# Kernel tuning notes

Hardware: AMD Instinct MI355X
Metric: run time of the kernel (lower is better)

Reference implementation:

```python
import math
import jax, jax.numpy as jnp
import numpy as np

N_LAYERS = 6
N_HEADS = 8
WINDOW = 4
LN_EPS = 1e-6


def _get_rel_emb(emb, length):
    # emb: [1, 2*WINDOW+1, kc] -> [1, 2*length-1, kc]
    max_rel = 2 * WINDOW + 1
    pad = max(0, length - (WINDOW + 1))
    start = max(0, WINDOW + 1 - length)
    end = max_rel + 2 * length - 1
    if pad > 0:
        emb = jnp.pad(emb, ((0, 0), (pad, pad), (0, 0)))
    return emb[:, start:end]


def _rel_to_abs(x):
    # x: [b,h,l,2l-1] -> [b,h,l,l]
    b, h, l, _ = x.shape
    x = jnp.pad(x, ((0, 0), (0, 0), (0, 0), (0, 1)))
    xf = x.reshape(b, h, l * 2 * l)
    xf = jnp.pad(xf, ((0, 0), (0, 0), (0, l - 1)))
    return xf.reshape(b, h, l + 1, 2 * l - 1)[:, :, :l, l - 1:]


def _abs_to_rel(x):
    # x: [b,h,l,l] -> [b,h,l,2l-1]
    b, h, l, _ = x.shape
    x = jnp.pad(x, ((0, 0), (0, 0), (0, 0), (0, l - 1)))
    xf = x.reshape(b, h, -1)
    xf = jnp.pad(xf, ((0, 0), (0, 0), (l, 0)))
    return xf.reshape(b, h, l, 2 * l)[..., 1:]


def _layer_norm(x, scale, bias):
    m = jnp.mean(x, axis=-1, keepdims=True)
    v = jnp.mean(jnp.square(x - m), axis=-1, keepdims=True)
    return (x - m) * jax.lax.rsqrt(v + LN_EPS) * scale + bias


def _forward(x, x_mask, Wq, bq, Wk, bk, Wv, bv, Wo, bo, emb_rel_k, emb_rel_v,
             ln1_scale, ln1_bias, W1, b1, W2, b2, ln2_scale, ln2_bias):
    B, T, C = x.shape
    H = N_HEADS
    KC = C // H
    scale = 1.0 / math.sqrt(KC)
    attn_mask = x_mask[:, :, None, :] * x_mask[:, :, :, None]  # [B,1,T,T]
    mask_t = jnp.transpose(x_mask, (0, 2, 1))  # [B,T,1]
    x = x * mask_t
    for l in range(N_LAYERS):
        # --- relative-position multi-head self-attention ---
        q = (x @ Wq[l] + bq[l]).reshape(B, T, H, KC).transpose(0, 2, 1, 3)
        k = (x @ Wk[l] + bk[l]).reshape(B, T, H, KC).transpose(0, 2, 1, 3)
        v = (x @ Wv[l] + bv[l]).reshape(B, T, H, KC).transpose(0, 2, 1, 3)
        scores = jnp.einsum('bhqd,bhkd->bhqk', q * scale, k)
        rk = _get_rel_emb(emb_rel_k[l], T)[0]  # [2T-1, KC] (heads shared)
        rel_logits = jnp.einsum('bhld,md->bhlm', q * scale, rk)
        scores = scores + _rel_to_abs(rel_logits)
        scores = jnp.where(attn_mask == 0, -10000.0, scores)
        p = jax.nn.softmax(scores, axis=-1)
        out = jnp.einsum('bhqk,bhkd->bhqd', p, v)
        rv = _get_rel_emb(emb_rel_v[l], T)[0]
        out = out + jnp.einsum('bhlm,md->bhld', _abs_to_rel(p), rv)
        out = out.transpose(0, 2, 1, 3).reshape(B, T, C)
        y = out @ Wo[l] + bo[l]
        x = _layer_norm(x + y, ln1_scale[l], ln1_bias[l])
        # --- pointwise conv FFN (kernel_size=1) ---
        h1 = jax.nn.relu((x * mask_t) @ W1[l] + b1[l])
        y = (h1 * mask_t) @ W2[l] + b2[l]
        y = y * mask_t
        x = _layer_norm(x + y, ln2_scale[l], ln2_bias[l])
    return x * mask_t


def setup_inputs() -> dict:
    key = jax.random.key(0)
    B, T, C, F, L, H = 8, 768, 512, 2048, N_LAYERS, N_HEADS
    KC = C // H
    ks = jax.random.split(key, 10)
    nrm = lambda k, s, sd=0.02: jax.random.normal(k, s, jnp.float32) * sd
    return {
        'x': jax.random.normal(ks[0], (B, T, C), jnp.float32),
        'x_mask': jnp.ones((B, 1, T), jnp.float32),
        'Wq': nrm(ks[1], (L, C, C)), 'bq': jnp.zeros((L, C), jnp.float32),
        'Wk': nrm(ks[2], (L, C, C)), 'bk': jnp.zeros((L, C), jnp.float32),
        'Wv': nrm(ks[3], (L, C, C)), 'bv': jnp.zeros((L, C), jnp.float32),
        'Wo': nrm(ks[4], (L, C, C)), 'bo': jnp.zeros((L, C), jnp.float32),
        'emb_rel_k': nrm(ks[5], (L, 1, 2 * WINDOW + 1, KC), KC ** -0.5),
        'emb_rel_v': nrm(ks[6], (L, 1, 2 * WINDOW + 1, KC), KC ** -0.5),
        'ln1_scale': jnp.ones((L, C), jnp.float32), 'ln1_bias': jnp.zeros((L, C), jnp.float32),
        'W1': nrm(ks[7], (L, C, F)), 'b1': jnp.zeros((L, F), jnp.float32),
        'W2': nrm(ks[8], (L, F, C)), 'b2': jnp.zeros((L, C), jnp.float32),
        'ln2_scale': jnp.ones((L, C), jnp.float32), 'ln2_bias': jnp.zeros((L, C), jnp.float32),
    }


def reference(x, x_mask, Wq, bq, Wk, bk, Wv, bv, Wo, bo, emb_rel_k, emb_rel_v,
              ln1_scale, ln1_bias, W1, b1, W2, b2, ln2_scale, ln2_bias):
    return _forward(x, x_mask, Wq, bq, Wk, bk, Wv, bv, Wo, bo, emb_rel_k, emb_rel_v,
                    ln1_scale, ln1_bias, W1, b1, W2, b2, ln2_scale, ln2_bias)
```

## Files before the change

### kernel.cpp

```cpp
#include <hip/hip_runtime.h>
#include <stdint.h>


typedef unsigned short u16;
typedef __attribute__((ext_vector_type(8))) __bf16 bf16x8;
typedef __attribute__((ext_vector_type(4))) float f32x4;

#define B_ 8
#define T_ 768
#define C_ 512
#define F_ 2048
#define LOG2E 1.4426950408889634f

__device__ __forceinline__ float b2f(u16 u) {
    union { float f; uint32_t i; } x; x.i = ((uint32_t)u) << 16; return x.f;
}
__device__ __forceinline__ u16 f2b(float f) {
    union { float f; uint32_t i; } x; x.f = f;
    return (u16)((x.i + 0x7fffu + ((x.i >> 16) & 1u)) >> 16);
}

template <int EPI>
__global__ __launch_bounds__(256) void gemm_bt4(
    const u16* __restrict__ A, int aStride,
    const u16* __restrict__ Bt, int bStride,
    const float* __restrict__ bias,
    u16* __restrict__ out, int oStride, int K, float epiScale)
{
    const int tid = threadIdx.x;
    const int wave = tid >> 6, lane = tid & 63;
    const int wm = wave & 1, wn = wave >> 1;
    const int quad = lane >> 4, l16 = lane & 15;
    const int m0 = blockIdx.x * 64;
    const int n0 = blockIdx.y * 64;

    __shared__ u16 As[64 * 64];
    __shared__ u16 Bs[64 * 64];

    const f32x4 vzero = {0.f, 0.f, 0.f, 0.f};
    f32x4 acc[2][2];
#pragma unroll
    for (int i = 0; i < 2; ++i)
#pragma unroll
        for (int j = 0; j < 2; ++j) acc[i][j] = vzero;

    for (int k0 = 0; k0 < K; k0 += 64) {
#pragma unroll
        for (int i = 0; i < 2; ++i) {
            int c = tid + i * 256;
            int row = c >> 3, pc = c & 7, lc = pc ^ (row & 7);
            *(uint4*)&As[c * 8] =
                *(const uint4*)(A + (long long)(m0 + row) * aStride + (k0 + lc * 8));
            *(uint4*)&Bs[c * 8] =
                *(const uint4*)(Bt + (long long)(n0 + row) * bStride + (k0 + lc * 8));
        }
        __syncthreads();
        __builtin_amdgcn_s_setprio(1);
#pragma unroll
        for (int ks = 0; ks < 2; ++ks) {
            bf16x8 af[2], bfr[2];
#pragma unroll
            for (int mi = 0; mi < 2; ++mi) {
                int row = wm * 32 + mi * 16 + l16;
                int pc = ((ks << 2) | quad) ^ (row & 7);
                af[mi] = *(const bf16x8*)&As[row * 64 + pc * 8];
            }
#pragma unroll
            for (int ni = 0; ni < 2; ++ni) {
                int row = wn * 32 + ni * 16 + l16;
                int pc = ((ks << 2) | quad) ^ (row & 7);
                bfr[ni] = *(const bf16x8*)&Bs[row * 64 + pc * 8];
            }
#pragma unroll
            for (int mi = 0; mi < 2; ++mi)
#pragma unroll
                for (int ni = 0; ni < 2; ++ni)
                    acc[mi][ni] = __builtin_amdgcn_mfma_f32_16x16x32_bf16(
                        bfr[ni], af[mi], acc[mi][ni], 0, 0, 0);
        }
        __builtin_amdgcn_s_setprio(0);
        __syncthreads();
    }

#pragma unroll
    for (int mi = 0; mi < 2; ++mi) {
        int row = m0 + wm * 32 + mi * 16 + l16;
#pragma unroll
        for (int ni = 0; ni < 2; ++ni) {
            int colb = n0 + wn * 32 + ni * 16 + quad * 4;
            u16 pk[4];
#pragma unroll
            for (int r = 0; r < 4; ++r) {
                float v = acc[mi][ni][r] + bias[colb + r];
                if (EPI == 1) v = v > 0.f ? v : 0.f;
                if (EPI == 3) { if (colb + r < 512) v *= epiScale; }
                pk[r] = f2b(v);
            }
            uint2 p;
            p.x = (uint32_t)pk[0] | ((uint32_t)pk[1] << 16);
            p.y = (uint32_t)pk[2] | ((uint32_t)pk[3] << 16);
            *(uint2*)(out + (long long)row * oStride + colb) = p;
        }
    }
}

__global__ __launch_bounds__(256) void bandg_k(
    const u16* __restrict__ qkv, const float* __restrict__ erk,
    float* __restrict__ bandg)
{
    __shared__ float erkS[576];
    const int tid = threadIdx.x;
    for (int idx = tid; idx < 576; idx += 256) erkS[idx] = erk[idx];
    __syncthreads();
    const int gid = blockIdx.x * 256 + tid;
    const int row = gid >> 3, h = gid & 7;
    const u16* q = qkv + (long long)row * 1536 + h * 64;
    float acc[9];
#pragma unroll
    for (int e = 0; e < 9; ++e) acc[e] = 0.f;
#pragma unroll
    for (int c = 0; c < 8; ++c) {
        uint4 d4 = *(const uint4*)(q + c * 8);
        const uint32_t dw[4] = {d4.x, d4.y, d4.z, d4.w};
#pragma unroll
        for (int j = 0; j < 8; ++j) {
            u16 uu = (u16)((dw[j >> 1] >> ((j & 1) * 16)) & 0xffff);
            float qv = b2f(uu);
            int d = c * 8 + j;
#pragma unroll
            for (int e = 0; e < 9; ++e) acc[e] += qv * erkS[e * 64 + d];
        }
    }
    float* o = bandg + (long long)gid * 9;
#pragma unroll
    for (int e = 0; e < 9; ++e) o[e] = acc[e];
}

__global__ __launch_bounds__(128) void flash_attn(
    const u16* __restrict__ qkv, const u16* __restrict__ vt,
    const float* __restrict__ mask, const float* __restrict__ bandg,
    const float* __restrict__ erv, u16* __restrict__ outb)
{
    const int tid = threadIdx.x;
    const int w = tid >> 6, lane = tid & 63;
    const int quad = lane >> 4, l16 = lane & 15;
    const int orig = blockIdx.y * 24 + blockIdx.x;
    const int swz = (orig & 7) * 192 + (orig >> 3);
    const int qt = swz % 24, bh = swz / 24;
    const int b = bh >> 3, h = bh & 7;
    const int q0 = qt * 32;

    __shared__ u16 Ql[32 * 64];
    __shared__ u16 Kt[64 * 64];
    __shared__ u16 Vt[64 * 64];
    __shared__ u16 Pl[2][16 * 64];
    __shared__ float bandk[32][10];
    __shared__ float maskK[64];

#pragma unroll
    for (int i = 0; i < 2; ++i) {
        int c = tid + i * 128;
        int r = c >> 3, pc = c & 7, lc = pc ^ (r & 7);
        *(uint4*)&Ql[c * 8] =
            *(const uint4*)(qkv + (long long)(b * T_ + q0 + r) * 1536 + h * 64 + lc * 8);
    }
    for (int idx = tid; idx < 288; idx += 128) {
        int r = idx / 9, e = idx - r * 9;
        bandk[r][e] = bandg[((long long)(b * T_ + q0 + r) * 8 + h) * 9 + e];
    }

    const int i_row = q0 + w * 16 + l16;
    const float mi = mask[b * T_ + i_row];
    float m_run = -1e30f, l_run = 0.f;
    const f32x4 vzero = {0.f, 0.f, 0.f, 0.f};
    f32x4 vacc[4] = {vzero, vzero, vzero, vzero};
    float pb[3] = {0.f, 0.f, 0.f};

    __syncthreads();
    bf16x8 qf[2];
#pragma unroll
    for (int ks = 0; ks < 2; ++ks) {
        int r = w * 16 + l16;
        int pc = ((ks << 2) | quad) ^ (r & 7);
        qf[ks] = *(const bf16x8*)&Ql[r * 64 + pc * 8];
    }

    for (int kt = 0; kt < 12; ++kt) {
        __syncthreads();
#pragma unroll
        for (int i = 0; i < 4; ++i) {
            int c = tid + i * 128;
            int r = c >> 3, pc = c & 7, lc = pc ^ (r & 7);
            *(uint4*)&Kt[c * 8] =
                *(const uint4*)(qkv + (long long)(b * T_ + kt * 64 + r) * 1536 + 512 + h * 64 + lc * 8);
            *(uint4*)&Vt[c * 8] =
                *(const uint4*)(vt + ((long long)bh * 64 + r) * T_ + kt * 64 + lc * 8);
        }
        if (tid < 64) maskK[tid] = mask[b * T_ + kt * 64 + tid];
        __syncthreads();

        const float mkv = maskK[lane];
        const bool tile_clean = (__ballot(mkv == 0.f) == 0ull);
        const bool fast = tile_clean && (mi != 0.f);
        const bool has_band = (kt * 64 <= q0 + w * 16 + 19) &&
                              (kt * 64 + 67 >= q0 + w * 16);

        f32x4 sacc[4];
#pragma unroll
        for (int ni = 0; ni < 4; ++ni) sacc[ni] = vzero;
        __builtin_amdgcn_s_setprio(1);
#pragma unroll
        for (int ks = 0; ks < 2; ++ks)
#pragma unroll
            for (int ni = 0; ni < 4; ++ni) {
                int r = ni * 16 + l16;
                int pc = ((ks << 2) | quad) ^ (r & 7);
                bf16x8 kf = *(const bf16x8*)&Kt[r * 64 + pc * 8];
                sacc[ni] = __builtin_amdgcn_mfma_f32_16x16x32_bf16(kf, qf[ks], sacc[ni], 0, 0, 0);
            }
        __builtin_amdgcn_s_setprio(0);

        if (has_band) {
#pragma unroll
            for (int ni = 0; ni < 4; ++ni)
#pragma unroll
                for (int r = 0; r < 4; ++r) {
                    int jl = ni * 16 + quad * 4 + r;
                    int dlt = kt * 64 + jl - i_row;
                    if (dlt >= -4 && dlt <= 4)
                        sacc[ni][r] += bandk[w * 16 + l16][dlt + 4];
                }
        }
        if (!fast) {
#pragma unroll
            for (int ni = 0; ni < 4; ++ni)
#pragma unroll
                for (int r = 0; r < 4; ++r) {
                    int jl = ni * 16 + quad * 4 + r;
                    if (mi * maskK[jl] == 0.f) sacc[ni][r] = -14427.0f;
                }
        }

        float mx;
        {
            float a0 = fmaxf(sacc[0][0], sacc[0][1]), a1 = fmaxf(sacc[0][2], sacc[0][3]);
            float b0 = fmaxf(sacc[1][0], sacc[1][1]), b1 = fmaxf(sacc[1][2], sacc[1][3]);
            float c0 = fmaxf(sacc[2][0], sacc[2][1]), c1 = fmaxf(sacc[2][2], sacc[2][3]);
            float d0 = fmaxf(sacc[3][0], sacc[3][1]), d1 = fmaxf(sacc[3][2], sacc[3][3]);
            float t0 = fmaxf(fmaxf(a0, a1), fmaxf(b0, b1));
            float t1 = fmaxf(fmaxf(c0, c1), fmaxf(d0, d1));
            mx = fmaxf(t0, t1);
        }
        mx = fmaxf(mx, __shfl_xor(mx, 16));
        mx = fmaxf(mx, __shfl_xor(mx, 32));
        const float m_new = fmaxf(m_run, mx);
        const float alpha = exp2f(m_run - m_new);
        m_run = m_new;
        l_run *= alpha;
#pragma unroll
        for (int ni = 0; ni < 4; ++ni) vacc[ni] = vacc[ni] * alpha;
#pragma unroll
        for (int k = 0; k < 3; ++k) pb[k] *= alpha;

        float lsum = 0.f;
#pragma unroll
        for (int ni = 0; ni < 4; ++ni) {
            float u0 = exp2f(sacc[ni][0] - m_new);
            float u1 = exp2f(sacc[ni][1] - m_new);
            float u2 = exp2f(sacc[ni][2] - m_new);
            float u3 = exp2f(sacc[ni][3] - m_new);
            lsum += (u0 + u1) + (u2 + u3);
            union { __bf16 h[2]; uint32_t u; } cA, cB;
            cA.h[0] = (__bf16)u0; cA.h[1] = (__bf16)u1;
            cB.h[0] = (__bf16)u2; cB.h[1] = (__bf16)u3;
            int c0 = ni * 16 + quad * 4;
            int phys = (((c0 >> 3) ^ (l16 & 7)) << 3) + (c0 & 7);
            uint2 p; p.x = cA.u; p.y = cB.u;
            *(uint2*)&Pl[w][l16 * 64 + phys] = p;
        }
        l_run += lsum;

        if (has_band) {
#pragma unroll
            for (int k = 0; k < 3; ++k) {
                int e = quad * 3 + k;
                if (e < 9) {
                    int jl = i_row + e - 4 - kt * 64;
                    if (jl >= 0 && jl < 64) {
                        int phys = (((jl >> 3) ^ (l16 & 7)) << 3) + (jl & 7);
                        pb[k] += b2f(Pl[w][l16 * 64 + phys]);
                    }
                }
            }
        }

        __builtin_amdgcn_s_setprio(1);
#pragma unroll
        for (int ks = 0; ks < 2; ++ks) {
            int pcc = ((ks << 2) | quad) ^ (l16 & 7);
            bf16x8 pf = *(const bf16x8*)&Pl[w][l16 * 64 + pcc * 8];
#pragma unroll
            for (int ni = 0; ni < 4; ++ni) {
                int r = ni * 16 + l16;
                int pc = ((ks << 2) | quad) ^ (r & 7);
                bf16x8 vf = *(const bf16x8*)&Vt[r * 64 + pc * 8];
                vacc[ni] = __builtin_amdgcn_mfma_f32_16x16x32_bf16(vf, pf, vacc[ni], 0, 0, 0);
            }
        }
        __builtin_amdgcn_s_setprio(0);
    }

    l_run += __shfl_xor(l_run, 16);
    l_run += __shfl_xor(l_run, 32);
    const float rinv = 1.f / l_run;

    float pband[9];
#pragma unroll
    for (int e = 0; e < 9; ++e) {
        float val = (quad == e / 3) ? pb[e % 3] : 0.f;
        val += __shfl_xor(val, 16);
        val += __shfl_xor(val, 32);
        pband[e] = val * rinv;
    }

    u16* orow = outb + (long long)(b * T_ + i_row) * C_ + h * 64;
#pragma unroll
    for (int ni = 0; ni < 4; ++ni) {
        u16 pk[4];
#pragma unroll
        for (int r = 0; r < 4; ++r) {
            int d = ni * 16 + quad * 4 + r;
            float v = vacc[ni][r] * rinv;
#pragma unroll
            for (int e = 0; e < 9; ++e) v += pband[e] * erv[e * 64 + d];
            pk[r] = f2b(v);
        }
        uint2 p;
        p.x = (uint32_t)pk[0] | ((uint32_t)pk[1] << 16);
        p.y = (uint32_t)pk[2] | ((uint32_t)pk[3] << 16);
        *(uint2*)(orow + ni * 16 + quad * 4) = p;
    }
}

__global__ void transpose_qkvo(const float* __restrict__ Wq, const float* __restrict__ Wk,
                               const float* __restrict__ Wv, const float* __restrict__ Wo,
                               u16* __restrict__ wqkvT, u16* __restrict__ woT)
{
    __shared__ u16 tile[32][33];
    const int z = blockIdx.z, l = z >> 2, which = z & 3;
    const float* src = (which == 0 ? Wq : which == 1 ? Wk : which == 2 ? Wv : Wo)
                       + (long long)l * 262144;
    u16* dst = (which == 3) ? woT + (long long)l * 262144
                            : wqkvT + (long long)l * 786432 + which * 262144;
    const int r0 = blockIdx.y * 32, c0 = blockIdx.x * 32;
    const int tx = threadIdx.x, ty = threadIdx.y;
#pragma unroll
    for (int i = 0; i < 32; i += 8)
        tile[ty + i][tx] = f2b(src[(long long)(r0 + ty + i) * 512 + (c0 + tx)]);
    __syncthreads();
#pragma unroll
    for (int i = 0; i < 32; i += 8)
        dst[(long long)(c0 + ty + i) * 512 + (r0 + tx)] = tile[tx][ty + i];
}

__global__ void transpose_f2bL(const float* __restrict__ src0, int sStride, long long sLayer,
                               u16* __restrict__ dst0, int dStride, long long dLayer)
{
    __shared__ u16 tile[32][33];
    const int l = blockIdx.z;
    const float* src = src0 + (long long)l * sLayer;
    u16* dst = dst0 + (long long)l * dLayer;
    const int r0 = blockIdx.y * 32, c0 = blockIdx.x * 32;
    const int tx = threadIdx.x, ty = threadIdx.y;
#pragma unroll
    for (int i = 0; i < 32; i += 8)
        tile[ty + i][tx] = f2b(src[(long long)(r0 + ty + i) * sStride + (c0 + tx)]);
    __syncthreads();
#pragma unroll
    for (int i = 0; i < 32; i += 8)
        dst[(long long)(c0 + ty + i) * dStride + (r0 + tx)] = tile[tx][ty + i];
}

__global__ void transpose_b(const u16* __restrict__ src, long long sB1, long long sB2, int sStride,
                            u16* __restrict__ dst, long long dB1, long long dB2, int dStride)
{
    __shared__ u16 tile[32][33];
    const int z = blockIdx.z, zb = z >> 3, zh = z & 7;
    src += (long long)zb * sB1 + (long long)zh * sB2;
    dst += (long long)zb * dB1 + (long long)zh * dB2;
    const int r0 = blockIdx.y * 32, c0 = blockIdx.x * 32;
    const int tx = threadIdx.x, ty = threadIdx.y;
#pragma unroll
    for (int i = 0; i < 32; i += 8)
        tile[ty + i][tx] = src[(long long)(r0 + ty + i) * sStride + (c0 + tx)];
    __syncthreads();
#pragma unroll
    for (int i = 0; i < 32; i += 8)
        dst[(long long)(c0 + ty + i) * dStride + (r0 + tx)] = tile[tx][ty + i];
}

__global__ void concat_bias(const float* __restrict__ bq, const float* __restrict__ bk,
                            const float* __restrict__ bv, float* __restrict__ dst)
{
    int i = blockIdx.x * 256 + threadIdx.x;
    int l = i / 1536, n = i - l * 1536;
    float v = (n < 512) ? bq[l * 512 + n]
             : (n < 1024 ? bk[l * 512 + (n - 512)] : bv[l * 512 + (n - 1024)]);
    dst[i] = v;
}

__global__ void mask_in(const float* __restrict__ x, const float* __restrict__ mask,
                        u16* __restrict__ out)
{
    int i4 = (blockIdx.x * 256 + threadIdx.x) * 4;
    float4 xv = *(const float4*)(x + i4);
    float m = mask[i4 >> 9];
    u16 pk[4] = {f2b(xv.x * m), f2b(xv.y * m), f2b(xv.z * m), f2b(xv.w * m)};
    uint2 p; p.x = (uint32_t)pk[0] | ((uint32_t)pk[1] << 16);
    p.y = (uint32_t)pk[2] | ((uint32_t)pk[3] << 16);
    *(uint2*)(out + i4) = p;
}

__global__ void mask_out(const u16* __restrict__ x, const float* __restrict__ mask,
                         float* __restrict__ out)
{
    int i4 = (blockIdx.x * 256 + threadIdx.x) * 4;
    uint2 p = *(const uint2*)(x + i4);
    float m = mask[i4 >> 9];
    float4 o;
    o.x = b2f((u16)(p.x & 0xffff)) * m;
    o.y = b2f((u16)(p.x >> 16)) * m;
    o.z = b2f((u16)(p.y & 0xffff)) * m;
    o.w = b2f((u16)(p.y >> 16)) * m;
    *(float4*)(out + i4) = o;
}

__global__ __launch_bounds__(256) void add_ln(
    const u16* __restrict__ x, const u16* __restrict__ y,
    const float* __restrict__ sc, const float* __restrict__ bi,
    u16* __restrict__ outx)
{
    const int wave = threadIdx.x >> 6, lane = threadIdx.x & 63;
    const long long r = (long long)blockIdx.x * 4 + wave;
    const u16* xr = x + r * C_;
    const u16* yr = y + r * C_;
    float v[8], s = 0.f;
#pragma unroll
    for (int it = 0; it < 2; ++it) {
        int j0 = it * 256 + lane * 4;
        uint2 px = *(const uint2*)(xr + j0);
        uint2 py = *(const uint2*)(yr + j0);
        v[it * 4 + 0] = b2f((u16)(px.x & 0xffff)) + b2f((u16)(py.x & 0xffff));
        v[it * 4 + 1] = b2f((u16)(px.x >> 16))    + b2f((u16)(py.x >> 16));
        v[it * 4 + 2] = b2f((u16)(px.y & 0xffff)) + b2f((u16)(py.y & 0xffff));
        v[it * 4 + 3] = b2f((u16)(px.y >> 16))    + b2f((u16)(py.y >> 16));
        s += v[it * 4 + 0] + v[it * 4 + 1] + v[it * 4 + 2] + v[it * 4 + 3];
    }
#pragma unroll
    for (int off = 32; off > 0; off >>= 1) s += __shfl_down(s, off);
    s = __shfl(s, 0);
    const float mean = s * (1.f / 512.f);
    float var = 0.f;
#pragma unroll
    for (int l = 0; l < 8; ++l) { float d = v[l] - mean; var += d * d; }
#pragma unroll
    for (int off = 32; off > 0; off >>= 1) var += __shfl_down(var, off);
    var = __shfl(var, 0);
    const float rs = rsqrtf(var * (1.f / 512.f) + 1e-6f);
    u16* orow = outx + r * C_;
#pragma unroll
    for (int it = 0; it < 2; ++it) {
        int j0 = it * 256 + lane * 4;
        float4 s4 = *(const float4*)(sc + j0);
        float4 b4 = *(const float4*)(bi + j0);
        u16 pk[4];
        pk[0] = f2b((v[it * 4 + 0] - mean) * rs * s4.x + b4.x);
        pk[1] = f2b((v[it * 4 + 1] - mean) * rs * s4.y + b4.y);
        pk[2] = f2b((v[it * 4 + 2] - mean) * rs * s4.z + b4.z);
        pk[3] = f2b((v[it * 4 + 3] - mean) * rs * s4.w + b4.w);
        uint2 p; p.x = (uint32_t)pk[0] | ((uint32_t)pk[1] << 16);
        p.y = (uint32_t)pk[2] | ((uint32_t)pk[3] << 16);
        *(uint2*)(orow + j0) = p;
    }
}

extern "C" void kernel_launch(void* const* d_in, const int* in_sizes, int n_in,
                              void* d_out, int out_size, void* d_ws, size_t ws_size,
                              hipStream_t stream)
{
    const float* x    = (const float*)d_in[0];
    const float* mask = (const float*)d_in[1];
    const float* Wq   = (const float*)d_in[2];
    const float* bq   = (const float*)d_in[3];
    const float* Wk   = (const float*)d_in[4];
    const float* bk   = (const float*)d_in[5];
    const float* Wv   = (const float*)d_in[6];
    const float* bv   = (const float*)d_in[7];
    const float* Wo   = (const float*)d_in[8];
    const float* bo   = (const float*)d_in[9];
    const float* erk  = (const float*)d_in[10];
    const float* erv  = (const float*)d_in[11];
    const float* ln1s = (const float*)d_in[12];
    const float* ln1b = (const float*)d_in[13];
    const float* W1   = (const float*)d_in[14];
    const float* b1   = (const float*)d_in[15];
    const float* W2   = (const float*)d_in[16];
    const float* b2   = (const float*)d_in[17];
    const float* ln2s = (const float*)d_in[18];
    const float* ln2b = (const float*)d_in[19];
    float* out = (float*)d_out;
    u16* ws  = (u16*)d_ws;

    const long long CF = 512LL * 2048;
    const int M = B_ * T_;

    u16* wqkvT   = ws;
    u16* woT     = ws + 4718592;
    u16* w1T     = ws + 6291456;
    u16* w2T     = ws + 12582912;
    float* bqkv  = (float*)(ws + 18874368);
    u16* xb      = ws + 18892800;
    u16* qkvb    = ws + 22038528;
    u16* vtb     = ws + 31475712;
    u16* attnb   = ws + 34621440;
    u16* scr     = ws + 37767168;
    float* bandg = (float*)(ws + 50350080);
    u16* yb      = vtb;

    const dim3 tb(32, 8);

    transpose_qkvo<<<dim3(16, 16, 24), tb, 0, stream>>>(Wq, Wk, Wv, Wo, wqkvT, woT);
    transpose_f2bL<<<dim3(64, 16, 6), tb, 0, stream>>>(W1, 2048, CF, w1T, 512, 1048576);
    transpose_f2bL<<<dim3(16, 64, 6), tb, 0, stream>>>(W2, 512,  CF, w2T, 2048, 1048576);
    concat_bias<<<36, 256, 0, stream>>>(bq, bk, bv, bqkv);
    mask_in<<<(M * 512) / 1024, 256, 0, stream>>>(x, mask, xb);

    for (int l = 0; l < 6; ++l) {
        gemm_bt4<3><<<dim3(96, 24), 256, 0, stream>>>(
            xb, 512, wqkvT + (long long)l * 786432, 512, bqkv + l * 1536,
            qkvb, 1536, 512, 0.125f * LOG2E);
        bandg_k<<<192, 256, 0, stream>>>(qkvb, erk + l * 576, bandg);
        transpose_b<<<dim3(2, 24, 64), tb, 0, stream>>>(
            qkvb + 1024, 768LL * 1536, 64, 1536,
            vtb, 8LL * 64 * 768, 64LL * 768, 768);
        flash_attn<<<dim3(24, 64), 128, 0, stream>>>(
            qkvb, vtb, mask, bandg, erv + l * 576, attnb);
        gemm_bt4<0><<<dim3(96, 8), 256, 0, stream>>>(
            attnb, 512, woT + (long long)l * 262144, 512, bo + l * 512,
            yb, 512, 512, 0.f);
        add_ln<<<1536, 256, 0, stream>>>(xb, yb, ln1s + l * 512, ln1b + l * 512, xb);
        gemm_bt4<1><<<dim3(96, 32), 256, 0, stream>>>(
            xb, 512, w1T + (long long)l * 1048576, 512, b1 + l * 2048,
            scr, 2048, 512, 0.f);
        gemm_bt4<0><<<dim3(96, 8), 256, 0, stream>>>(
            scr, 2048, w2T + (long long)l * 1048576, 2048, b2 + l * 512,
            yb, 512, 2048, 0.f);
        add_ln<<<1536, 256, 0, stream>>>(xb, yb, ln2s + l * 512, ln2b + l * 512, xb);
    }

    mask_out<<<(M * 512) / 1024, 256, 0, stream>>>(xb, mask, out);
}
```

Baseline: 1.017 ms.

## Load K/V fragments directly from global memory in single-wave attention blocks

The attention kernel changes from two-wave blocks that stage K and V tiles in shared memory to one-wave blocks of 16 query rows. Each lane reads its K and V MFMA fragments straight from global memory, which removes the per-tile block barriers and LDS copies. The cost is that each K/V tile is fetched twice as often, once per 16-row block instead of once per 32 rows, so the kernel leans on L2/L1 cache hits. Row-mask handling now uses a wave ballot, and mask values go to LDS only on the slow path.

```diff
diff --git a/kernel.cpp b/kernel.cpp
--- a/kernel.cpp
+++ b/kernel.cpp
@@ -136,74 +136,60 @@
     for (int e = 0; e < 9; ++e) o[e] = acc[e];
 }
 
-__global__ __launch_bounds__(128) void flash_attn(
+__global__ __launch_bounds__(64) void flash_attn(
     const u16* __restrict__ qkv, const u16* __restrict__ vt,
     const float* __restrict__ mask, const float* __restrict__ bandg,
     const float* __restrict__ erv, u16* __restrict__ outb)
 {
-    const int tid = threadIdx.x;
-    const int w = tid >> 6, lane = tid & 63;
+    const int lane = threadIdx.x;
     const int quad = lane >> 4, l16 = lane & 15;
-    const int orig = blockIdx.y * 24 + blockIdx.x;
-    const int swz = (orig & 7) * 192 + (orig >> 3);
-    const int qt = swz % 24, bh = swz / 24;
+    const int orig = blockIdx.y * 48 + blockIdx.x;
+    const int swz = (orig & 7) * 384 + (orig >> 3);
+    const int qt = swz % 48, bh = swz / 48;
     const int b = bh >> 3, h = bh & 7;
-    const int q0 = qt * 32;
-
-    __shared__ u16 Ql[32 * 64];
-    __shared__ u16 Kt[64 * 64];
-    __shared__ u16 Vt[64 * 64];
-    __shared__ u16 Pl[2][16 * 64];
-    __shared__ float bandk[32][10];
-    __shared__ float maskK[64];
-
-#pragma unroll
-    for (int i = 0; i < 2; ++i) {
-        int c = tid + i * 128;
-        int r = c >> 3, pc = c & 7, lc = pc ^ (r & 7);
-        *(uint4*)&Ql[c * 8] =
-            *(const uint4*)(qkv + (long long)(b * T_ + q0 + r) * 1536 + h * 64 + lc * 8);
-    }
-    for (int idx = tid; idx < 288; idx += 128) {
+    const int q0 = qt * 16;
+
+    __shared__ u16 Pl[16 * 64];
+    __shared__ float bandk[16][10];
+    __shared__ float maskW[64];
+
+    for (int idx = lane; idx < 144; idx += 64) {
         int r = idx / 9, e = idx - r * 9;
         bandk[r][e] = bandg[((long long)(b * T_ + q0 + r) * 8 + h) * 9 + e];
     }
-
-    const int i_row = q0 + w * 16 + l16;
+    __syncthreads();
+
+    const int i_row = q0 + l16;
     const float mi = mask[b * T_ + i_row];
+    const bool row_masked_any = (__ballot(mi == 0.f) != 0ull);
+
+    const u16* qrow = qkv + (long long)(b * T_ + i_row) * 1536 + h * 64;
+    bf16x8 qf[2];
+#pragma unroll
+    for (int ks = 0; ks < 2; ++ks)
+        qf[ks] = *(const bf16x8*)(qrow + ks * 32 + quad * 8);
+
+    const u16* kbase[4];
+    const u16* vbase[4];
+#pragma unroll
+    for (int ni = 0; ni < 4; ++ni) {
+        int r = ni * 16 + l16;
+        kbase[ni] = qkv + ((long long)(b * T_) + r) * 1536 + 512 + h * 64;
+        vbase[ni] = vt + ((long long)bh * 64 + r) * T_;
+    }
+
     float m_run = -1e30f, l_run = 0.f;
     const f32x4 vzero = {0.f, 0.f, 0.f, 0.f};
     f32x4 vacc[4] = {vzero, vzero, vzero, vzero};
     float pb[3] = {0.f, 0.f, 0.f};
 
-    __syncthreads();
-    bf16x8 qf[2];
-#pragma unroll
-    for (int ks = 0; ks < 2; ++ks) {
-        int r = w * 16 + l16;
-        int pc = ((ks << 2) | quad) ^ (r & 7);
-        qf[ks] = *(const bf16x8*)&Ql[r * 64 + pc * 8];
-    }
-
     for (int kt = 0; kt < 12; ++kt) {
-        __syncthreads();
-#pragma unroll
-        for (int i = 0; i < 4; ++i) {
-            int c = tid + i * 128;
-            int r = c >> 3, pc = c & 7, lc = pc ^ (r & 7);
-            *(uint4*)&Kt[c * 8] =
-                *(const uint4*)(qkv + (long long)(b * T_ + kt * 64 + r) * 1536 + 512 + h * 64 + lc * 8);
-            *(uint4*)&Vt[c * 8] =
-                *(const uint4*)(vt + ((long long)bh * 64 + r) * T_ + kt * 64 + lc * 8);
-        }
-        if (tid < 64) maskK[tid] = mask[b * T_ + kt * 64 + tid];
-        __syncthreads();
-
-        const float mkv = maskK[lane];
-        const bool tile_clean = (__ballot(mkv == 0.f) == 0ull);
-        const bool fast = tile_clean && (mi != 0.f);
-        const bool has_band = (kt * 64 <= q0 + w * 16 + 19) &&
-                              (kt * 64 + 67 >= q0 + w * 16);
+        const float mval = mask[b * T_ + kt * 64 + lane];
+        const bool tile_clean = (__ballot(mval == 0.f) == 0ull);
+        const bool fast = tile_clean && !row_masked_any;
+        const bool has_band = (kt * 64 <= q0 + 19) && (kt * 64 + 67 >= q0);
+        const long long ktoff = (long long)kt * 64 * 1536;
+        const int kcol = quad * 8;
 
         f32x4 sacc[4];
 #pragma unroll
@@ -213,9 +199,7 @@
         for (int ks = 0; ks < 2; ++ks)
 #pragma unroll
             for (int ni = 0; ni < 4; ++ni) {
-                int r = ni * 16 + l16;
-                int pc = ((ks << 2) | quad) ^ (r & 7);
-                bf16x8 kf = *(const bf16x8*)&Kt[r * 64 + pc * 8];
+                bf16x8 kf = *(const bf16x8*)(kbase[ni] + ktoff + ks * 32 + kcol);
                 sacc[ni] = __builtin_amdgcn_mfma_f32_16x16x32_bf16(kf, qf[ks], sacc[ni], 0, 0, 0);
             }
         __builtin_amdgcn_s_setprio(0);
@@ -228,16 +212,17 @@
                     int jl = ni * 16 + quad * 4 + r;
                     int dlt = kt * 64 + jl - i_row;
                     if (dlt >= -4 && dlt <= 4)
-                        sacc[ni][r] += bandk[w * 16 + l16][dlt + 4];
+                        sacc[ni][r] += bandk[l16][dlt + 4];
                 }
         }
         if (!fast) {
+            maskW[lane] = mval;
 #pragma unroll
             for (int ni = 0; ni < 4; ++ni)
 #pragma unroll
                 for (int r = 0; r < 4; ++r) {
                     int jl = ni * 16 + quad * 4 + r;
-                    if (mi * maskK[jl] == 0.f) sacc[ni][r] = -14427.0f;
+                    if (mi * maskW[jl] == 0.f) sacc[ni][r] = -14427.0f;
                 }
         }
 
@@ -270,13 +255,13 @@
             float u2 = exp2f(sacc[ni][2] - m_new);
             float u3 = exp2f(sacc[ni][3] - m_new);
             lsum += (u0 + u1) + (u2 + u3);
-            union { __bf16 h[2]; uint32_t u; } cA, cB;
-            cA.h[0] = (__bf16)u0; cA.h[1] = (__bf16)u1;
-            cB.h[0] = (__bf16)u2; cB.h[1] = (__bf16)u3;
+            union { __bf16 hh[2]; uint32_t u; } cA, cB;
+            cA.hh[0] = (__bf16)u0; cA.hh[1] = (__bf16)u1;
+            cB.hh[0] = (__bf16)u2; cB.hh[1] = (__bf16)u3;
             int c0 = ni * 16 + quad * 4;
             int phys = (((c0 >> 3) ^ (l16 & 7)) << 3) + (c0 & 7);
             uint2 p; p.x = cA.u; p.y = cB.u;
-            *(uint2*)&Pl[w][l16 * 64 + phys] = p;
+            *(uint2*)&Pl[l16 * 64 + phys] = p;
         }
         l_run += lsum;
 
@@ -288,7 +273,7 @@
                     int jl = i_row + e - 4 - kt * 64;
                     if (jl >= 0 && jl < 64) {
                         int phys = (((jl >> 3) ^ (l16 & 7)) << 3) + (jl & 7);
-                        pb[k] += b2f(Pl[w][l16 * 64 + phys]);
+                        pb[k] += b2f(Pl[l16 * 64 + phys]);
                     }
                 }
             }
@@ -298,12 +283,10 @@
 #pragma unroll
         for (int ks = 0; ks < 2; ++ks) {
             int pcc = ((ks << 2) | quad) ^ (l16 & 7);
-            bf16x8 pf = *(const bf16x8*)&Pl[w][l16 * 64 + pcc * 8];
+            bf16x8 pf = *(const bf16x8*)&Pl[l16 * 64 + pcc * 8];
 #pragma unroll
             for (int ni = 0; ni < 4; ++ni) {
-                int r = ni * 16 + l16;
-                int pc = ((ks << 2) | quad) ^ (r & 7);
-                bf16x8 vf = *(const bf16x8*)&Vt[r * 64 + pc * 8];
+                bf16x8 vf = *(const bf16x8*)(vbase[ni] + kt * 64 + ks * 32 + kcol);
                 vacc[ni] = __builtin_amdgcn_mfma_f32_16x16x32_bf16(vf, pf, vacc[ni], 0, 0, 0);
             }
         }
@@ -543,7 +526,7 @@
         transpose_b<<<dim3(2, 24, 64), tb, 0, stream>>>(
             qkvb + 1024, 768LL * 1536, 64, 1536,
             vtb, 8LL * 64 * 768, 64LL * 768, 768);
-        flash_attn<<<dim3(24, 64), 128, 0, stream>>>(
+        flash_attn<<<dim3(48, 64), 64, 0, stream>>>(
             qkvb, vtb, mask, bandg, erv + l * 576, attnb);
         gemm_bt4<0><<<dim3(96, 8), 256, 0, stream>>>(
             attnb, 512, woT + (long long)l * 262144, 512, bo + l * 512,
```

Measured after the change: 1.379 ms. +35.5%, slower.
